# Kernel tuning notes

Measured on AMD Instinct MI355X. Metric: run time of the kernel, lower is better.

The kernel has to match this reference:

```python
import jax, jax.numpy as jnp
import numpy as np

T = 3072          # packed tokens (B==1 varlen)
DIM = 1024        # model_dim
H = 8             # num_heads
D = 128           # head_dim
GATE_IN = 16      # gate projections read first 16 channels of x
ATTN_SCALE = 0.1  # Yarn attn_scale
BM = 1408         # sliding-window size (block_size * ws)


def _rms_norm(x, eps=1e-6):
    return x * jax.lax.rsqrt(jnp.mean(x * x, axis=-1, keepdims=True) + eps)


def _rotary(x, cos, sin):
    # x: [B,T,H,D]; cos/sin: [T,D//2]
    c = cos[None, :x.shape[1], None, :]
    s = sin[None, :x.shape[1], None, :]
    x1, x2 = jnp.split(x, 2, axis=-1)
    return jnp.concatenate([x1 * c + x2 * s, -x1 * s + x2 * c], axis=-1)


def setup_inputs() -> dict:
    key = jax.random.key(0)
    ks = jax.random.split(key, 6)
    x = jax.random.normal(ks[0], (1, T, DIM), dtype=jnp.float32)
    qkvo_w = 0.02 * jax.random.normal(ks[1], (4 * DIM, DIM), dtype=jnp.float32)
    sa_lambdas = jnp.ones((2,), dtype=jnp.float32)
    ve = 0.5 * jax.random.normal(ks[2], (T, DIM), dtype=jnp.float32)
    attn_gate_w = 0.1 * jax.random.normal(ks[3], (H, GATE_IN), dtype=jnp.float32)
    ve_gate_w = 0.1 * jax.random.normal(ks[4], (H, GATE_IN), dtype=jnp.float32)
    # Yarn rotary tables: half the freq channels are zero (NoPE half)
    angular_freq = (1.0 / 1024.0) ** jnp.linspace(0, 1, D // 4, dtype=jnp.float32)
    angular_freq = jnp.concatenate([angular_freq, jnp.zeros(D // 4, dtype=jnp.float32)])
    theta = jnp.arange(T, dtype=jnp.float32)[:, None] * angular_freq[None, :]
    cos, sin = jnp.cos(theta), jnp.sin(theta)
    # two packed sequences of length T//2 (cu_seqlens = [0, T//2, T])
    seg_ids = jnp.concatenate([jnp.zeros(T // 2, jnp.int32), jnp.ones(T // 2, jnp.int32)])
    return {"x": x, "qkvo_w": qkvo_w, "sa_lambdas": sa_lambdas, "ve": ve,
            "attn_gate_w": attn_gate_w, "ve_gate_w": ve_gate_w,
            "cos": cos, "sin": sin, "seg_ids": seg_ids, "bm_size": BM}


def reference(x, qkvo_w, sa_lambdas, ve, attn_gate_w, ve_gate_w, cos, sin, seg_ids, bm_size):
    B, Tt, dim = x.shape
    nh = attn_gate_w.shape[0]
    hd = dim // nh
    # fused qkv projection with learned lambda scaling
    qkv = x @ (sa_lambdas[0] * qkvo_w[:3 * dim]).T              # [B,T,3*dim]
    qkv = qkv.reshape(B, Tt, 3 * nh, hd)
    q, k, v = jnp.split(qkv, 3, axis=2)                          # each [B,T,H,D]
    q, k = _rms_norm(q), _rms_norm(k)
    q, k = _rotary(q, cos, sin), _rotary(k, cos, sin)
    # key_offset: channels [D/4:D/2] and [3D/4:D] take previous token's keys
    k_prev = jnp.concatenate([k[:, :1], k[:, :-1]], axis=1)
    k = jnp.concatenate([k[..., :hd // 4], k_prev[..., hd // 4:hd // 2],
                         k[..., hd // 2:3 * hd // 4], k_prev[..., 3 * hd // 4:]], axis=-1)
    # value-embedding gate: 2*sigmoid(x[:,:,:16] @ W^T)
    ve_gate = 2.0 * jax.nn.sigmoid(x[..., :ve_gate_w.shape[-1]] @ ve_gate_w.T)  # [B,T,H]
    v = v + ve_gate[..., None] * ve.reshape(B, Tt, nh, hd)
    # windowed causal varlen attention (dense reference for flash_attn_varlen)
    scores = jnp.einsum('bthd,bshd->bhts', q, k) * ATTN_SCALE
    t_idx = jnp.arange(Tt)
    mask = ((t_idx[None, :] <= t_idx[:, None])
            & (t_idx[None, :] >= t_idx[:, None] - bm_size)
            & (seg_ids[None, :] == seg_ids[:, None]))
    scores = jnp.where(mask[None, None], scores, -jnp.inf)
    p = jax.nn.softmax(scores, axis=-1)
    y = jnp.einsum('bhts,bshd->bthd', p, v)
    # attention output gate
    gate = jax.nn.sigmoid(x[..., :attn_gate_w.shape[-1]] @ attn_gate_w.T)      # [B,T,H]
    y = y * gate[..., None]
    y = y.reshape(B, Tt, dim)
    return y @ (sa_lambdas[1] * qkvo_w[3 * dim:]).T
```

## Files before the change

### kernel.cpp

```cpp
#include <hip/hip_runtime.h>
#include <hip/hip_bf16.h>
#include <stdint.h>

#define TSEQ 3072
#define DIMM 1024
#define NH   8
#define HD   128
#define QBLK 32
#define BM   1408
#define CHUNK 384
#define NQB  (TSEQ / QBLK)
#define NCMAX 5

typedef float f32x4 __attribute__((ext_vector_type(4)));
typedef short s16x8 __attribute__((ext_vector_type(8)));
typedef unsigned short u16;

static __device__ __forceinline__ u16 f2b(float f) {
  union { float f; unsigned u; } a; a.f = f;
  unsigned r = a.u + 0x7FFFu + ((a.u >> 16) & 1u);
  return (u16)(r >> 16);
}
static __device__ __forceinline__ float b2f(u16 u) {
  union { unsigned u; float f; } a; a.u = ((unsigned)u) << 16;
  return a.f;
}
static __device__ __forceinline__ void gload_lds16(const void* g, void* l) {
  __builtin_amdgcn_global_load_lds(
      (const __attribute__((address_space(1))) unsigned int*)(unsigned long long)g,
      (__attribute__((address_space(3))) unsigned int*)(unsigned long long)l,
      16, 0, 0);
}
static __device__ __forceinline__ void bar() {
  asm volatile("" ::: "memory");
  __builtin_amdgcn_s_barrier();
  asm volatile("" ::: "memory");
}
#define SWAIT(n) asm volatile("s_waitcnt vmcnt(" #n ")" ::: "memory")

__global__ __launch_bounds__(256) void k_convert(
    const float* __restrict__ x, const float* __restrict__ w,
    const float* __restrict__ lam,
    u16* __restrict__ xb, u16* __restrict__ wb)
{
  const int NX = TSEQ * DIMM;
  const int NW = 4 * DIMM * DIMM;
  const float l0 = lam[0], l1 = lam[1];
  const int n4 = (NX + NW) >> 2;
  for (int j = blockIdx.x * 256 + threadIdx.x; j < n4; j += gridDim.x * 256) {
    const int e = j << 2;
    float4 v; u16* dst; float s;
    if (e < NX) { v = *(const float4*)(x + e); dst = xb + e; s = 1.f; }
    else {
      const int we = e - NX;
      v = *(const float4*)(w + we);
      dst = wb + we;
      s = (we < 3 * DIMM * DIMM) ? l0 : l1;
    }
    dst[0] = f2b(v.x * s); dst[1] = f2b(v.y * s);
    dst[2] = f2b(v.z * s); dst[3] = f2b(v.w * s);
  }
}

__global__ __launch_bounds__(256) void k_gemm_nt(
    const u16* __restrict__ A, const u16* __restrict__ B,
    float* __restrict__ C, int M, int N, int K)
{
  __shared__ u16 As[128 * 64];
  __shared__ u16 Bs[128 * 64];
  const int tid = threadIdx.x;
  const int lane = tid & 63, wv = tid >> 6;
  const int m0 = blockIdx.y * 128, n0 = blockIdx.x * 128;
  const int wm = (wv >> 1) * 64, wn = (wv & 1) * 64;
  const int c0 = lane & 15, r0 = (lane >> 4) * 4, koff = (lane >> 4) * 8;

  f32x4 acc[4][4];
  #pragma unroll
  for (int i = 0; i < 4; i++)
    #pragma unroll
    for (int j = 0; j < 4; j++) acc[i][j] = (f32x4){0.f, 0.f, 0.f, 0.f};

  const int srow = tid >> 3;
  const int scol = (tid & 7) * 8;
  const size_t a_base = (size_t)(m0 + srow) * K + scol;
  const size_t b_base = (size_t)(n0 + srow) * K + scol;

  for (int kt = 0; kt < K; kt += 64) {
    __syncthreads();
    #pragma unroll
    for (int i = 0; i < 4; i++) {
      gload_lds16(A + a_base + (size_t)(i * 32) * K + kt, (char*)As + i * 4096 + tid * 16);
      gload_lds16(B + b_base + (size_t)(i * 32) * K + kt, (char*)Bs + i * 4096 + tid * 16);
    }
    __syncthreads();
    #pragma unroll
    for (int kk = 0; kk < 2; kk++) {
      s16x8 af[4], bf[4];
      #pragma unroll
      for (int i = 0; i < 4; i++) {
        af[i] = *(const s16x8*)&As[(wm + i * 16 + c0) * 64 + kk * 32 + koff];
        bf[i] = *(const s16x8*)&Bs[(wn + i * 16 + c0) * 64 + kk * 32 + koff];
      }
      #pragma unroll
      for (int i = 0; i < 4; i++)
        #pragma unroll
        for (int j = 0; j < 4; j++)
          acc[i][j] = __builtin_amdgcn_mfma_f32_16x16x32_bf16(af[i], bf[j], acc[i][j], 0, 0, 0);
    }
  }
  #pragma unroll
  for (int i = 0; i < 4; i++)
    #pragma unroll
    for (int j = 0; j < 4; j++) {
      float* cp = C + (size_t)(m0 + wm + i * 16 + r0) * N + n0 + wn + j * 16 + c0;
      #pragma unroll
      for (int r = 0; r < 4; r++) cp[(size_t)r * N] = acc[i][j][r];
    }
}

__global__ __launch_bounds__(256) void k_prep(
    const float* __restrict__ qkv, const float* __restrict__ x,
    const float* __restrict__ ve, const float* __restrict__ cosb,
    const float* __restrict__ sinb, const float* __restrict__ gwa,
    const float* __restrict__ gwv, const int* __restrict__ seg,
    u16* __restrict__ Qg, u16* __restrict__ Kg, u16* __restrict__ VTg,
    float* __restrict__ gateA, int* __restrict__ segb)
{
  __shared__ u16 vtile[64][130];
  const int tid = threadIdx.x;
  const int lane = tid & 63, w = tid >> 6;
  const int h = blockIdx.y;
  const int t0 = blockIdx.x * 64;

  if (h == 0 && t0 == 0 && tid == 0) {
    const int sv = seg[0];
    int lo = 1, hi = TSEQ;
    while (lo < hi) { const int mid = (lo + hi) >> 1; if (seg[mid] == sv) lo = mid + 1; else hi = mid; }
    segb[0] = lo;
  }

  for (int it = 0; it < 16; ++it) {
    const int tt = it * 4 + w;
    const int t = t0 + tt;
    const int tp = (t == 0) ? 0 : t - 1;

    const float* qrow = qkv + (size_t)t * (3 * DIMM) + h * HD;
    const float* krow = qrow + DIMM;
    const float* vrow = qrow + 2 * DIMM;
    const float* prow = qkv + (size_t)tp * (3 * DIMM) + DIMM + h * HD;

    float q1 = qrow[lane], q2 = qrow[lane + 64];
    float k1 = krow[lane], k2 = krow[lane + 64];
    float p1 = prow[lane], p2 = prow[lane + 64];

    float sq = q1 * q1 + q2 * q2, sk = k1 * k1 + k2 * k2, sp = p1 * p1 + p2 * p2;
    #pragma unroll
    for (int m = 1; m < 64; m <<= 1) {
      sq += __shfl_xor(sq, m, 64);
      sk += __shfl_xor(sk, m, 64);
      sp += __shfl_xor(sp, m, 64);
    }
    const float rq = rsqrtf(sq * (1.f / 128.f) + 1e-6f);
    const float rk = rsqrtf(sk * (1.f / 128.f) + 1e-6f);
    const float rp = rsqrtf(sp * (1.f / 128.f) + 1e-6f);
    q1 *= rq; q2 *= rq; k1 *= rk; k2 *= rk; p1 *= rp; p2 *= rp;

    const float c  = cosb[t * 64 + lane],  s  = sinb[t * 64 + lane];
    const float cp = cosb[tp * 64 + lane], spv = sinb[tp * 64 + lane];
    const float qo1 =  q1 * c + q2 * s,   qo2 = -q1 * s + q2 * c;
    const float ko1 =  k1 * c + k2 * s,   ko2 = -k1 * s + k2 * c;
    const float po1 =  p1 * cp + p2 * spv, po2 = -p1 * spv + p2 * cp;
    const float m1 = (lane < 32) ? ko1 : po1;
    const float m2 = (lane < 32) ? ko2 : po2;

    const size_t qkbase = ((size_t)h * TSEQ + t) * HD + lane;
    Qg[qkbase] = f2b(qo1 * 0.1f); Qg[qkbase + 64] = f2b(qo2 * 0.1f);
    Kg[qkbase] = f2b(m1);  Kg[qkbase + 64] = f2b(m2);

    float dv = 0.f, da = 0.f;
    #pragma unroll
    for (int g = 0; g < 16; g++) {
      const float xv = x[(size_t)t * DIMM + g];
      dv += xv * gwv[h * 16 + g];
      da += xv * gwa[h * 16 + g];
    }
    const float vg = 2.f / (1.f + __expf(-dv));
    const float v1 = vrow[lane]      + vg * ve[(size_t)t * DIMM + h * HD + lane];
    const float v2 = vrow[lane + 64] + vg * ve[(size_t)t * DIMM + h * HD + lane + 64];
    vtile[tt][lane] = f2b(v1); vtile[tt][lane + 64] = f2b(v2);
    if (lane == 0) gateA[h * TSEQ + t] = 1.f / (1.f + __expf(-da));
  }
  __syncthreads();
  #pragma unroll
  for (int rep = 0; rep < 4; ++rep) {
    const int d = rep * 32 + (tid >> 3);
    const int cc = (tid & 7) * 8;
    s16x8 v;
    #pragma unroll
    for (int j = 0; j < 8; j++) ((u16*)&v)[j] = vtile[cc + j][d];
    *(s16x8*)(VTg + ((size_t)h * HD + d) * TSEQ + t0 + cc) = v;
  }
}

__global__ __launch_bounds__(128) void k_attn(
    const u16* __restrict__ Qg, const u16* __restrict__ Kg,
    const u16* __restrict__ VTg, const int* __restrict__ segb,
    u16* __restrict__ Opart, float* __restrict__ Mp, float* __restrict__ Lp)
{
  __shared__ u16 Ks[2][64 * HD];
  __shared__ u16 Vs[HD * 64];
  __shared__ u16 Ps[2][16 * 64];

  const int h  = blockIdx.x;
  const int qb = blockIdx.y;
  const int rc = blockIdx.z;
  const int q0 = qb * QBLK;

  const int c_lo = ((q0 - BM) > 0 ? (q0 - BM) : 0) / CHUNK;
  const int c_hi = (q0 + QBLK - 1) / CHUNK;
  if (rc > c_hi - c_lo) return;
  const int c = c_lo + rc;

  const int tid = threadIdx.x, lane = tid & 63, wv = tid >> 6;
  const int qw = q0 + wv * 16;
  const int r0 = (lane >> 4) * 4, c0 = lane & 15;
  const int koff = (lane >> 4) * 8;

  const int b = segb[0];

  int loop_lo = q0 - BM; if (loop_lo < 0) loop_lo = 0;
  if (q0 >= b) loop_lo = (loop_lo > b) ? loop_lo : b;
  int s_lo = loop_lo & ~63;
  const int cs = c * CHUNK;
  if (s_lo < cs) s_lo = cs;
  int s_hi = q0 + QBLK;
  if (s_hi > cs + CHUNK) s_hi = cs + CHUNK;

  s16x8 qf[4];
  {
    const u16* qp = Qg + ((size_t)h * TSEQ + qw + c0) * HD + koff;
    #pragma unroll
    for (int kk = 0; kk < 4; kk++) qf[kk] = *(const s16x8*)(qp + kk * 32);
  }

  int qt[4]; int qub[4];
  #pragma unroll
  for (int r = 0; r < 4; r++) { qt[r] = qw + r0 + r; qub[r] = (qt[r] >= b) ? 1 : 0; }

  f32x4 o[8];
  #pragma unroll
  for (int i = 0; i < 8; i++) o[i] = (f32x4){0.f, 0.f, 0.f, 0.f};
  float mrow[4] = {-1e30f, -1e30f, -1e30f, -1e30f};
  float lrow[4] = {0.f, 0.f, 0.f, 0.f};

  auto stageK = [&](int buf, int s0k) {
    #pragma unroll
    for (int i = 0; i < 8; i++) {
      const int L = tid * 16 + i * 2048;
      const int kr = L >> 8;
      const int kc = (L & 255) ^ ((kr & 7) << 4);
      gload_lds16(Kg + ((size_t)h * TSEQ + s0k + kr) * HD + (kc >> 1), (char*)Ks[buf] + L);
    }
  };
  auto stageV = [&](int s0v) {
    #pragma unroll
    for (int i = 0; i < 8; i++) {
      const int L = tid * 16 + i * 2048;
      const int vr = L >> 7;
      const int vc = (L & 127) ^ ((vr & 7) << 4);
      gload_lds16(VTg + ((size_t)h * HD + vr) * TSEQ + s0v + (vc >> 1), (char*)Vs + L);
    }
  };

  if (s_lo < s_hi) {
    stageK(0, s_lo);
    int cur = 0;
    for (int s0 = s_lo; s0 < s_hi; s0 += 64) {
      bar();
      stageV(s0);
      int sn = s0 + 64; if (sn >= s_hi) sn = s0;
      stageK(cur ^ 1, sn);
      SWAIT(16);
      bar();

      const char* kbase = (const char*)Ks[cur];
      f32x4 sv[4];
      #pragma unroll
      for (int n = 0; n < 4; n++) {
        sv[n] = (f32x4){0.f, 0.f, 0.f, 0.f};
        const int krow = n * 16 + c0;
        #pragma unroll
        for (int kk = 0; kk < 4; kk++) {
          const int kbyte = (krow << 8) + ((((kk * 32 + koff) << 1)) ^ ((krow & 7) << 4));
          const s16x8 kf = *(const s16x8*)(kbase + kbyte);
          sv[n] = __builtin_amdgcn_mfma_f32_16x16x32_bf16(qf[kk], kf, sv[n], 0, 0, 0);
        }
      }

      const bool keys_same_seg_as_q =
          ((s0 >= b) && (qw >= b)) || ((s0 + 63 < b) && (qw + 15 < b));
      const bool interior = (s0 + 64 <= qw) && (s0 >= qw + 15 - BM) && keys_same_seg_as_q;
      if (!interior) {
        #pragma unroll
        for (int n = 0; n < 4; n++) {
          const int key = s0 + n * 16 + c0;
          const int kub = (key >= b) ? 1 : 0;
          #pragma unroll
          for (int r = 0; r < 4; r++) {
            const bool ok = (key <= qt[r]) && (key >= qt[r] - BM) && (kub == qub[r]);
            sv[n][r] = ok ? sv[n][r] : -1e30f;
          }
        }
      }

      float pm[4];
      #pragma unroll
      for (int r = 0; r < 4; r++)
        pm[r] = fmaxf(fmaxf(sv[0][r], sv[1][r]), fmaxf(sv[2][r], sv[3][r]));
      #pragma unroll
      for (int m = 1; m < 16; m <<= 1)
        #pragma unroll
        for (int r = 0; r < 4; r++) pm[r] = fmaxf(pm[r], __shfl_xor(pm[r], m, 64));

      int need = 0;
      #pragma unroll
      for (int r = 0; r < 4; r++) need |= (pm[r] > mrow[r] + 8.f) ? 1 : 0;
      if (__any(need)) {
        #pragma unroll
        for (int r = 0; r < 4; r++) {
          const float mn = fmaxf(mrow[r], pm[r]);
          const float scl = __expf(mrow[r] - mn);
          mrow[r] = mn;
          lrow[r] *= scl;
          #pragma unroll
          for (int i = 0; i < 8; i++) o[i][r] *= scl;
        }
      }

      u16 pb[4][4];
      #pragma unroll
      for (int n = 0; n < 4; n++)
        #pragma unroll
        for (int r = 0; r < 4; r++) {
          const float p = (sv[n][r] < -0.5e30f) ? 0.f : __expf(sv[n][r] - mrow[r]);
          lrow[r] += p;
          pb[n][r] = f2b(p);
        }

      char* pbase = (char*)Ps[wv];
      #pragma unroll
      for (int n = 0; n < 4; n++)
        #pragma unroll
        for (int r = 0; r < 4; r++) {
          const int row = r0 + r;
          const int byt = (row << 7) + ((((n * 16 + c0) << 1)) ^ ((row & 7) << 4));
          *(u16*)(pbase + byt) = pb[n][r];
        }

      SWAIT(8);
      bar();

      #pragma unroll
      for (int kc = 0; kc < 2; kc++) {
        const int pbyte = (c0 << 7) + ((((kc * 32 + koff) << 1)) ^ ((c0 & 7) << 4));
        const s16x8 pf = *(const s16x8*)(pbase + pbyte);
        #pragma unroll
        for (int nf = 0; nf < 8; nf++) {
          const int vrow = nf * 16 + c0;
          const int vbyte = (vrow << 7) + ((((kc * 32 + koff) << 1)) ^ ((vrow & 7) << 4));
          const s16x8 vf = *(const s16x8*)((const char*)Vs + vbyte);
          o[nf] = __builtin_amdgcn_mfma_f32_16x16x32_bf16(pf, vf, o[nf], 0, 0, 0);
        }
      }
      cur ^= 1;
    }
    SWAIT(0);
  }

  #pragma unroll
  for (int m = 1; m < 16; m <<= 1)
    #pragma unroll
    for (int r = 0; r < 4; r++) lrow[r] += __shfl_xor(lrow[r], m, 64);

  const int pidx = (h * NQB + qb) * NCMAX + rc;
  #pragma unroll
  for (int r = 0; r < 4; r++) {
    const int wrow = wv * 16 + r0 + r;
    u16* op = Opart + (size_t)pidx * (32 * 128) + wrow * 128;
    #pragma unroll
    for (int nf = 0; nf < 8; nf++) op[nf * 16 + c0] = f2b(o[nf][r]);
    if (c0 == 0) {
      Mp[pidx * 32 + wrow] = mrow[r];
      Lp[pidx * 32 + wrow] = lrow[r];
    }
  }
}

__global__ __launch_bounds__(256) void k_merge(
    const u16* __restrict__ Opart, const float* __restrict__ Mp,
    const float* __restrict__ Lp, const float* __restrict__ gateA,
    u16* __restrict__ Y)
{
  const int qb = blockIdx.x, h = blockIdx.y;
  const int q0 = qb * QBLK;
  const int c_lo = ((q0 - BM) > 0 ? (q0 - BM) : 0) / CHUNK;
  const int c_hi = (q0 + QBLK - 1) / CHUNK;
  const int nc = c_hi - c_lo + 1;

  const int tid = threadIdx.x;
  const int row = tid >> 3;
  const int dg = (tid & 7) * 16;
  const int qt = q0 + row;
  const int base = (h * NQB + qb) * NCMAX;

  float m = -1e30f;
  for (int rc = 0; rc < nc; rc++) {
    const float mc = Mp[(base + rc) * 32 + row];
    m = fmaxf(m, mc);
  }
  float l = 0.f;
  float acc[16];
  #pragma unroll
  for (int j = 0; j < 16; j++) acc[j] = 0.f;
  for (int rc = 0; rc < nc; rc++) {
    const float mc = Mp[(base + rc) * 32 + row];
    const float w = __expf(mc - m);
    l += w * Lp[(base + rc) * 32 + row];
    const u16* op = Opart + (size_t)(base + rc) * (32 * 128) + row * 128 + dg;
    const s16x8 v0 = *(const s16x8*)(op);
    const s16x8 v1 = *(const s16x8*)(op + 8);
    #pragma unroll
    for (int j = 0; j < 8; j++) {
      acc[j]     += w * b2f(((const u16*)&v0)[j]);
      acc[j + 8] += w * b2f(((const u16*)&v1)[j]);
    }
  }
  const float inv = (l > 0.f) ? (gateA[h * TSEQ + qt] / l) : 0.f;
  u16* yp = Y + (size_t)qt * DIMM + h * HD + dg;
  #pragma unroll
  for (int j = 0; j < 16; j++) yp[j] = f2b(acc[j] * inv);
}

extern "C" void kernel_launch(void* const* d_in, const int* in_sizes, int n_in,
                              void* d_out, int out_size, void* d_ws, size_t ws_size,
                              hipStream_t stream) {
  const float* x    = (const float*)d_in[0];
  const float* qkvo = (const float*)d_in[1];
  const float* lam  = (const float*)d_in[2];
  const float* ve   = (const float*)d_in[3];
  const float* gwa  = (const float*)d_in[4];
  const float* gwv  = (const float*)d_in[5];
  const float* cosb = (const float*)d_in[6];
  const float* sinb = (const float*)d_in[7];
  const int*   seg  = (const int*)d_in[8];
  float* out = (float*)d_out;

  char* ws = (char*)d_ws;
  size_t off = 0;
  auto alloc = [&](size_t bytes) -> void* {
    void* p = ws + off;
    off += (bytes + 255) & ~(size_t)255;
    return p;
  };
  u16*   xb    = (u16*)alloc((size_t)TSEQ * DIMM * 2);
  u16*   wb    = (u16*)alloc((size_t)4 * DIMM * DIMM * 2);
  float* qkv   = (float*)alloc((size_t)TSEQ * 3 * DIMM * 4);
  u16*   Qg    = (u16*)alloc((size_t)NH * TSEQ * HD * 2);
  u16*   Kg    = (u16*)alloc((size_t)NH * TSEQ * HD * 2);
  u16*   VTg   = (u16*)alloc((size_t)NH * HD * TSEQ * 2);
  float* gateA = (float*)alloc((size_t)NH * TSEQ * 4);
  u16*   Yg    = (u16*)alloc((size_t)TSEQ * DIMM * 2);
  int*   segb  = (int*)alloc(256);

  u16*   Opart = (u16*)qkv;
  float* Mp    = (float*)((char*)qkv + (size_t)NH * NQB * NCMAX * 32 * 128 * 2);
  float* Lp    = Mp + (size_t)NH * NQB * NCMAX * 32;

  k_convert<<<2048, 256, 0, stream>>>(x, qkvo, lam, xb, wb);
  k_gemm_nt<<<dim3(24, 24), 256, 0, stream>>>(xb, wb, qkv, TSEQ, 3 * DIMM, DIMM);
  k_prep<<<dim3(TSEQ / 64, NH), 256, 0, stream>>>(qkv, x, ve, cosb, sinb, gwa, gwv, seg,
                                                  Qg, Kg, VTg, gateA, segb);
  k_attn<<<dim3(NH, NQB, NCMAX), 128, 0, stream>>>(Qg, Kg, VTg, segb, Opart, Mp, Lp);
  k_merge<<<dim3(NQB, NH), 256, 0, stream>>>(Opart, Mp, Lp, gateA, Yg);
  k_gemm_nt<<<dim3(DIMM / 128, 24), 256, 0, stream>>>(Yg, wb + (size_t)3 * DIMM * DIMM, out, TSEQ, DIMM, DIMM);
}
```

Before: 239.8 us.

## Double-buffer GEMM LDS tiles with XOR swizzle to overlap loads and MFMA

The NT GEMM now uses two LDS buffers and issues the next K-tile's global-to-LDS loads before computing on the current tile, waiting with counted vmcnt instead of full barriers around the loads. It also XOR-swizzles the LDS column layout by row to cut bank conflicts on the fragment reads. This aims to hide global load latency and LDS conflicts in the projection GEMMs, at the cost of doubled LDS use, which may lower occupancy.

```diff
diff --git a/kernel.cpp b/kernel.cpp
--- a/kernel.cpp
+++ b/kernel.cpp
@@ -66,8 +66,8 @@
     const u16* __restrict__ A, const u16* __restrict__ B,
     float* __restrict__ C, int M, int N, int K)
 {
-  __shared__ u16 As[128 * 64];
-  __shared__ u16 Bs[128 * 64];
+  __shared__ u16 As[2][128 * 64];
+  __shared__ u16 Bs[2][128 * 64];
   const int tid = threadIdx.x;
   const int lane = tid & 63, wv = tid >> 6;
   const int m0 = blockIdx.y * 128, n0 = blockIdx.x * 128;
@@ -80,26 +80,41 @@
     #pragma unroll
     for (int j = 0; j < 4; j++) acc[i][j] = (f32x4){0.f, 0.f, 0.f, 0.f};
 
-  const int srow = tid >> 3;
-  const int scol = (tid & 7) * 8;
-  const size_t a_base = (size_t)(m0 + srow) * K + scol;
-  const size_t b_base = (size_t)(n0 + srow) * K + scol;
-
+  const int srow  = tid >> 3;
+  const int scolb = (tid & 7) * 16;
+
+  auto stage = [&](int buf, int kt) {
+    #pragma unroll
+    for (int i = 0; i < 4; i++) {
+      const int row = srow + i * 32;
+      const int scb = scolb ^ ((row & 7) << 4);
+      const int ldst = row * 128 + scolb;
+      gload_lds16(A + (size_t)(m0 + row) * K + kt + (scb >> 1), (char*)As[buf] + ldst);
+      gload_lds16(B + (size_t)(n0 + row) * K + kt + (scb >> 1), (char*)Bs[buf] + ldst);
+    }
+  };
+
+  stage(0, 0);
+  int cur = 0;
   for (int kt = 0; kt < K; kt += 64) {
-    __syncthreads();
-    #pragma unroll
-    for (int i = 0; i < 4; i++) {
-      gload_lds16(A + a_base + (size_t)(i * 32) * K + kt, (char*)As + i * 4096 + tid * 16);
-      gload_lds16(B + b_base + (size_t)(i * 32) * K + kt, (char*)Bs + i * 4096 + tid * 16);
-    }
-    __syncthreads();
+    if (kt + 64 < K) {
+      stage(cur ^ 1, kt + 64);
+      SWAIT(8);
+    } else {
+      SWAIT(0);
+    }
+    bar();
+
     #pragma unroll
     for (int kk = 0; kk < 2; kk++) {
       s16x8 af[4], bf[4];
       #pragma unroll
       for (int i = 0; i < 4; i++) {
-        af[i] = *(const s16x8*)&As[(wm + i * 16 + c0) * 64 + kk * 32 + koff];
-        bf[i] = *(const s16x8*)&Bs[(wn + i * 16 + c0) * 64 + kk * 32 + koff];
+        const int ar = wm + i * 16 + c0;
+        const int br = wn + i * 16 + c0;
+        const int cb = (kk * 32 + koff) * 2;
+        af[i] = *(const s16x8*)((const char*)As[cur] + ar * 128 + (cb ^ ((ar & 7) << 4)));
+        bf[i] = *(const s16x8*)((const char*)Bs[cur] + br * 128 + (cb ^ ((br & 7) << 4)));
       }
       #pragma unroll
       for (int i = 0; i < 4; i++)
@@ -107,7 +122,11 @@
         for (int j = 0; j < 4; j++)
           acc[i][j] = __builtin_amdgcn_mfma_f32_16x16x32_bf16(af[i], bf[j], acc[i][j], 0, 0, 0);
     }
-  }
+
+    bar();
+    cur ^= 1;
+  }
+
   #pragma unroll
   for (int i = 0; i < 4; i++)
     #pragma unroll
```

Measured after the change: 209.9 us. -12.5%, faster.
